# Kernel tuning notes

Measured on AMD Instinct MI355X. Metric: run time of the kernel, lower is better.

The kernel has to match this reference:

```python
import jax, jax.numpy as jnp
import numpy as np

E = 512      # embedding_size
H = 8        # heads
FF = 4 * E   # ffn hidden
EPS = 1e-5


def layer_norm(x, gamma, beta):
    mu = jnp.mean(x, axis=-1, keepdims=True)
    var = jnp.mean((x - mu) ** 2, axis=-1, keepdims=True)
    return (x - mu) * jax.lax.rsqrt(var + EPS) * gamma + beta


def setup_inputs() -> dict:
    key = jax.random.key(0)
    ks = jax.random.split(key, 12)
    N, L = 4, 2048
    s = E ** -0.5
    return {
        "x": jax.random.normal(ks[0], (N, L, E), jnp.float32),
        "wq": jax.random.normal(ks[1], (E, E), jnp.float32) * s,
        "wk": jax.random.normal(ks[2], (E, E), jnp.float32) * s,
        "wv": jax.random.normal(ks[3], (E, E), jnp.float32) * s,
        "wo": jax.random.normal(ks[4], (E, E), jnp.float32) * s,
        "bo": jnp.zeros((E,), jnp.float32),
        "g1": jnp.ones((E,), jnp.float32),
        "b1": jnp.zeros((E,), jnp.float32),
        "g2": jnp.ones((E,), jnp.float32),
        "b2": jnp.zeros((E,), jnp.float32),
        "w1": jax.random.normal(ks[5], (E, FF), jnp.float32) * s,
        "bf1": jnp.zeros((FF,), jnp.float32),
        "w2": jax.random.normal(ks[6], (FF, E), jnp.float32) * (FF ** -0.5),
        "bf2": jnp.zeros((E,), jnp.float32),
    }


def reference(x, wq, wk, wv, wo, bo, g1, b1, g2, b2, w1, bf1, w2, bf2):
    N, L, _ = x.shape
    skip = x
    h = layer_norm(x, g1, b1)
    # attention (weights stored as [in, out])
    q = (h @ wq).reshape(N, L, H, E // H)
    k = (h @ wk).reshape(N, L, H, E // H)
    v = (h @ wv).reshape(N, L, H, E // H)
    # NOTE: source scales by embedding_size**-0.5 (not head_dim)
    scores = jnp.einsum('nqhd,nkhd->nhqk', q, k) * (E ** -0.5)
    attn = jax.nn.softmax(scores, axis=-1)
    out = jnp.einsum('nhql,nlhd->nqhd', attn, v).reshape(N, L, E)
    x = out @ wo + bo + skip
    skip = x
    h = layer_norm(x, g2, b2)  # dropout is identity in eval
    h = jax.nn.silu(h @ w1 + bf1) @ w2 + bf2
    return h + skip
```

## Files before the change

kernel.cpp:

```cpp
#include <hip/hip_runtime.h>
#include <hip/hip_bf16.h>

typedef __bf16 bf16;
typedef __attribute__((ext_vector_type(2))) __bf16 bf16x2;
typedef __attribute__((ext_vector_type(8))) __bf16 bf16x8;
typedef __attribute__((ext_vector_type(4))) float f32x4;
typedef __attribute__((ext_vector_type(16))) float f32x16;

#define MFMA16(a, b, c) __builtin_amdgcn_mfma_f32_16x16x32_bf16((a), (b), (c), 0, 0, 0)
#define MFMA32(a, b, c) __builtin_amdgcn_mfma_f32_32x32x16_bf16((a), (b), (c), 0, 0, 0)


__device__ __forceinline__ void load_lds16(const bf16* g, bf16* l) {
    __builtin_amdgcn_global_load_lds(
        (const __attribute__((address_space(1))) void*)g,
        (__attribute__((address_space(3))) void*)l, 16, 0, 0);
}

__device__ __forceinline__ float fexp2(float x) { return __builtin_amdgcn_exp2f(x); }

__global__ void cvt_all(const float* __restrict__ wq, const float* __restrict__ wk,
                        const float* __restrict__ wv, const float* __restrict__ wo,
                        const float* __restrict__ w1, const float* __restrict__ w2,
                        bf16* __restrict__ wqkv_t, bf16* __restrict__ wo_t,
                        bf16* __restrict__ w1_t, bf16* __restrict__ w2_t) {
    __shared__ float t[64][65];
    const int b = blockIdx.x;
    const float* src; bf16* dst;
    int sstride, dstride, r0, c0, dr0;
    if (b < 192) {
        int bx = b % 24, by = b / 24;
        int j0 = bx * 64;
        src = (j0 < 512) ? wq : (j0 < 1024) ? wk : wv;
        sstride = 512; r0 = by * 64; c0 = j0 & 511;
        dst = wqkv_t; dstride = 512; dr0 = j0;
    } else if (b < 256) {
        int tt = b - 192; int bx = tt % 8, by = tt / 8;
        src = wo; sstride = 512; r0 = by * 64; c0 = bx * 64;
        dst = wo_t; dstride = 512; dr0 = c0;
    } else if (b < 512) {
        int tt = b - 256; int bx = tt % 32, by = tt / 32;
        src = w1; sstride = 2048; r0 = by * 64; c0 = bx * 64;
        dst = w1_t; dstride = 512; dr0 = c0;
    } else {
        int tt = b - 512; int bx = tt % 8, by = tt / 8;
        src = w2; sstride = 512; r0 = by * 64; c0 = bx * 64;
        dst = w2_t; dstride = 2048; dr0 = c0;
    }
    #pragma unroll
    for (int p = 0; p < 16; p++) {
        int lin = threadIdx.x + p * 256;
        int rr = lin >> 6, cc = lin & 63;
        t[rr][cc] = src[(size_t)(r0 + rr) * sstride + c0 + cc];
    }
    __syncthreads();
    #pragma unroll
    for (int p = 0; p < 16; p++) {
        int lin = threadIdx.x + p * 256;
        int cc = lin >> 6, rr = lin & 63;
        dst[(size_t)(dr0 + cc) * dstride + r0 + rr] = (bf16)t[rr][cc];
    }
}

__global__ void ln_kernel(const float* __restrict__ x, const float* __restrict__ g,
                          const float* __restrict__ b, bf16* __restrict__ out) {
    int row = blockIdx.x * 4 + (threadIdx.x >> 6);
    int lane = threadIdx.x & 63;
    const float4* xr = (const float4*)(x + (size_t)row * 512);
    float4 v0 = xr[lane];
    float4 v1 = xr[lane + 64];
    float s  = v0.x + v0.y + v0.z + v0.w + v1.x + v1.y + v1.z + v1.w;
    float sq = v0.x*v0.x + v0.y*v0.y + v0.z*v0.z + v0.w*v0.w
             + v1.x*v1.x + v1.y*v1.y + v1.z*v1.z + v1.w*v1.w;
    #pragma unroll
    for (int d = 1; d < 64; d <<= 1) { s += __shfl_xor(s, d); sq += __shfl_xor(sq, d); }
    float mean = s * (1.f / 512.f);
    float var  = sq * (1.f / 512.f) - mean * mean;
    float rs   = rsqrtf(var + 1e-5f);
    const float4* gv = (const float4*)g;
    const float4* bv = (const float4*)b;
    float4 ga = gv[lane], gb = gv[lane + 64];
    float4 ba = bv[lane], bb = bv[lane + 64];
    bf16* orow = out + (size_t)row * 512;
    int c0 = lane * 4;
    orow[c0 + 0]   = (bf16)((v0.x - mean) * rs * ga.x + ba.x);
    orow[c0 + 1]   = (bf16)((v0.y - mean) * rs * ga.y + ba.y);
    orow[c0 + 2]   = (bf16)((v0.z - mean) * rs * ga.z + ba.z);
    orow[c0 + 3]   = (bf16)((v0.w - mean) * rs * ga.w + ba.w);
    orow[c0 + 256] = (bf16)((v1.x - mean) * rs * gb.x + bb.x);
    orow[c0 + 257] = (bf16)((v1.y - mean) * rs * gb.y + bb.y);
    orow[c0 + 258] = (bf16)((v1.z - mean) * rs * gb.z + bb.z);
    orow[c0 + 259] = (bf16)((v1.w - mean) * rs * gb.w + bb.w);
}

template<int KD, int ND, int EPI>
__global__ __launch_bounds__(256, 3) void gemm_k(
        const bf16* __restrict__ A, const bf16* __restrict__ Bt,
        const float* __restrict__ bias, void* __restrict__ outp) {
    __shared__ bf16 As[128 * 64];
    __shared__ bf16 Bs[128 * 64];
    const int bm = blockIdx.x, bn = blockIdx.y;
    const int tid = threadIdx.x;
    const int w = tid >> 6, lane = tid & 63;
    const int wm = (w >> 1) * 64, wn = (w & 1) * 64;
    const int lr = lane & 15, lq = lane >> 4, lr7 = lane & 7;
    const int srow = lane >> 3, gslot = lane & 7;
    f32x4 acc[4][4] = {};
    const bf16* Ab = A + (size_t)bm * 128 * KD;
    const bf16* Bb = Bt + (size_t)bn * 128 * KD;
    const int gcol = (gslot ^ srow) * 8;
    for (int k0 = 0; k0 < KD; k0 += 64) {
        __syncthreads();
        #pragma unroll
        for (int s = 0; s < 4; s++) {
            int rbase = w * 32 + s * 8;
            int row = rbase + srow;
            load_lds16(&Ab[(size_t)row * KD + k0 + gcol], &As[rbase * 64]);
            load_lds16(&Bb[(size_t)row * KD + k0 + gcol], &Bs[rbase * 64]);
        }
        __syncthreads();
        #pragma unroll
        for (int ks = 0; ks < 2; ks++) {
            bf16x8 af[4], bfr[4];
            #pragma unroll
            for (int mi = 0; mi < 4; mi++) {
                int row = wm + mi * 16 + lr;
                af[mi] = *(const bf16x8*)&As[row * 64 + (((ks * 4 + lq) ^ lr7) << 3)];
            }
            #pragma unroll
            for (int ni = 0; ni < 4; ni++) {
                int row = wn + ni * 16 + lr;
                bfr[ni] = *(const bf16x8*)&Bs[row * 64 + (((ks * 4 + lq) ^ lr7) << 3)];
            }
            #pragma unroll
            for (int mi = 0; mi < 4; mi++)
                #pragma unroll
                for (int ni = 0; ni < 4; ni++)
                    acc[mi][ni] = MFMA16(af[mi], bfr[ni], acc[mi][ni]);
        }
    }
    #pragma unroll
    for (int mi = 0; mi < 4; mi++)
        #pragma unroll
        for (int ni = 0; ni < 4; ni++)
            #pragma unroll
            for (int r = 0; r < 4; r++) {
                int row = bm * 128 + wm + mi * 16 + lq * 4 + r;
                int col = bn * 128 + wn + ni * 16 + lr;
                float v = acc[mi][ni][r];
                size_t off = (size_t)row * ND + col;
                if constexpr (EPI == 0) {
                    ((bf16*)outp)[off] = (bf16)v;
                } else {
                    v += bias[col];
                    v = v / (1.f + __expf(-v));
                    ((bf16*)outp)[off] = (bf16)v;
                }
            }
}

template<int KD>
__global__ __launch_bounds__(256, 4) void gemm64(
        const bf16* __restrict__ A, const bf16* __restrict__ Bt,
        const float* __restrict__ bias, const float* __restrict__ resid,
        float* __restrict__ outp) {
    __shared__ bf16 As[64 * 64];
    __shared__ bf16 Bs[64 * 64];
    const int bm = blockIdx.x, bn = blockIdx.y;
    const int tid = threadIdx.x;
    const int w = tid >> 6, lane = tid & 63;
    const int wm = (w >> 1) * 32, wn = (w & 1) * 32;
    const int lr = lane & 15, lq = lane >> 4, lr7 = lane & 7;
    const int srow = lane >> 3, gslot = lane & 7;
    f32x4 acc[2][2] = {};
    const bf16* Ab = A + (size_t)bm * 64 * KD;
    const bf16* Bb = Bt + (size_t)bn * 64 * KD;
    const int gcol = (gslot ^ srow) * 8;
    for (int k0 = 0; k0 < KD; k0 += 64) {
        __syncthreads();
        #pragma unroll
        for (int s = 0; s < 2; s++) {
            int rbase = w * 16 + s * 8;
            int row = rbase + srow;
            load_lds16(&Ab[(size_t)row * KD + k0 + gcol], &As[rbase * 64]);
            load_lds16(&Bb[(size_t)row * KD + k0 + gcol], &Bs[rbase * 64]);
        }
        __syncthreads();
        #pragma unroll
        for (int ks = 0; ks < 2; ks++) {
            bf16x8 af[2], bfr[2];
            #pragma unroll
            for (int mi = 0; mi < 2; mi++) {
                int row = wm + mi * 16 + lr;
                af[mi] = *(const bf16x8*)&As[row * 64 + (((ks * 4 + lq) ^ lr7) << 3)];
            }
            #pragma unroll
            for (int ni = 0; ni < 2; ni++) {
                int row = wn + ni * 16 + lr;
                bfr[ni] = *(const bf16x8*)&Bs[row * 64 + (((ks * 4 + lq) ^ lr7) << 3)];
            }
            #pragma unroll
            for (int mi = 0; mi < 2; mi++)
                #pragma unroll
                for (int ni = 0; ni < 2; ni++)
                    acc[mi][ni] = MFMA16(af[mi], bfr[ni], acc[mi][ni]);
        }
    }
    #pragma unroll
    for (int mi = 0; mi < 2; mi++)
        #pragma unroll
        for (int ni = 0; ni < 2; ni++)
            #pragma unroll
            for (int r = 0; r < 4; r++) {
                int row = bm * 64 + wm + mi * 16 + lq * 4 + r;
                int col = bn * 64 + wn + ni * 16 + lr;
                size_t off = (size_t)row * 512 + col;
                outp[off] = acc[mi][ni][r] + bias[col] + resid[off];
            }
}

__global__ void vt_kernel(const bf16* __restrict__ qkvb, bf16* __restrict__ Vt) {
    __shared__ bf16 t[64 * 72];
    const int nh = blockIdx.x & 31, lt = blockIdx.x >> 5;
    const int n = nh >> 3, h = nh & 7;
    const int tid = threadIdx.x;
    #pragma unroll
    for (int p = 0; p < 2; p++) {
        int lin = tid + p * 256;
        int rr = lin >> 3, cc = lin & 7;
        bf16x8 v = *(const bf16x8*)&qkvb[(size_t)(n * 2048 + lt * 64 + rr) * 1536
                                         + 1024 + h * 64 + cc * 8];
        *(bf16x8*)&t[rr * 72 + (cc ^ (rr & 7)) * 8] = v;
    }
    __syncthreads();
    #pragma unroll
    for (int p = 0; p < 2; p++) {
        int lin = tid + p * 256;
        int dd = lin & 63, llc = lin >> 6;
        bf16x8 o;
        #pragma unroll
        for (int j = 0; j < 8; j++) {
            int ll = llc * 8 + j;
            o[j] = t[ll * 72 + (((dd >> 3) ^ (ll & 7)) * 8) + (dd & 7)];
        }
        *(bf16x8*)&Vt[(size_t)(nh * 64 + dd) * 2048 + lt * 64 + llc * 8] = o;
    }
}

__global__ __launch_bounds__(512, 4) void attn_kernel(const bf16* __restrict__ qkv,
                                                      const bf16* __restrict__ Vt,
                                                      bf16* __restrict__ aout) {
    __shared__ float accbuf[4][32][64];
    __shared__ float psumbuf[4][32];
    __shared__ bf16 Ot[4][32 * 72];
    const int b = blockIdx.x;
    const int nh = b & 31;
    const int qt = b >> 5;
    const int n = nh >> 3, h = nh & 7;
    const int tid = threadIdx.x, w = tid >> 6, lane = tid & 63;
    const int qsub = w & 3, ks = w >> 2;
    const int lq5 = lane & 31, g = lane >> 5;
    const float cf = 0.04419417382415922f * 1.4426950408889634f;

    const bf16* Qp = qkv + (size_t)(n * 2048 + qt * 128 + qsub * 32 + lq5) * 1536
                     + h * 64 + g * 8;
    bf16x8 qf[4];
    #pragma unroll
    for (int c = 0; c < 4; c++) {
        bf16x8 raw = *(const bf16x8*)(Qp + c * 16);
        #pragma unroll
        for (int j = 0; j < 8; j++) qf[c][j] = (bf16)((float)raw[j] * cf);
    }

    f32x16 acc0 = {0}, acc1 = {0};
    float psum = 0.f;

    const bf16* Kp = qkv + (size_t)(n * 2048 + ks * 1024 + lq5) * 1536
                     + 512 + h * 64 + g * 8;
    const bf16* Vp = Vt + (size_t)(nh * 64 + lq5) * 2048 + ks * 1024 + g * 8;

    bf16x8 kfn[4];
    kfn[0] = *(const bf16x8*)(Kp);
    kfn[1] = *(const bf16x8*)(Kp + 16);
    kfn[2] = *(const bf16x8*)(Kp + 32);
    kfn[3] = *(const bf16x8*)(Kp + 48);

    #pragma unroll 2
    for (int t = 0; t < 32; t++) {
        const bf16* Vc = Vp + t * 32;
        bf16x8 v00 = *(const bf16x8*)(Vc);
        bf16x8 v01 = *(const bf16x8*)(Vc + (size_t)32 * 2048);
        bf16x8 v10 = *(const bf16x8*)(Vc + 16);
        bf16x8 v11 = *(const bf16x8*)(Vc + 16 + (size_t)32 * 2048);

        f32x16 st = {0};
        st = MFMA32(kfn[0], qf[0], st);
        st = MFMA32(kfn[1], qf[1], st);
        st = MFMA32(kfn[2], qf[2], st);
        st = MFMA32(kfn[3], qf[3], st);

        if (t < 31) {
            const bf16* Kt = Kp + (size_t)(t + 1) * 32 * 1536;
            kfn[0] = *(const bf16x8*)(Kt);
            kfn[1] = *(const bf16x8*)(Kt + 16);
            kfn[2] = *(const bf16x8*)(Kt + 32);
            kfn[3] = *(const bf16x8*)(Kt + 48);
        }

        #pragma unroll
        for (int h16 = 0; h16 < 2; h16++) {
            uint32_t pk[4];
            #pragma unroll
            for (int i = 0; i < 4; i++) {
                float p0 = fexp2(fminf(st[8 * h16 + 2 * i], 60.f));
                float p1 = fexp2(fminf(st[8 * h16 + 2 * i + 1], 60.f));
                psum += p0 + p1;
                union { uint32_t u; bf16x2 hh; } cvu;
                cvu.hh = bf16x2{(bf16)p0, (bf16)p1};
                pk[i] = cvu.u;
            }
            uint32_t s0 = g ? pk[0] : pk[2];
            uint32_t s1 = g ? pk[1] : pk[3];
            uint32_t r0 = (uint32_t)__shfl_xor((int)s0, 32);
            uint32_t r1 = (uint32_t)__shfl_xor((int)s1, 32);
            union { uint4 u; bf16x8 v; } pf;
            pf.u = g == 0 ? uint4{pk[0], pk[1], r0, r1}
                          : uint4{r0, r1, pk[2], pk[3]};
            if (h16 == 0) {
                acc0 = MFMA32(v00, pf.v, acc0);
                acc1 = MFMA32(v01, pf.v, acc1);
            } else {
                acc0 = MFMA32(v10, pf.v, acc0);
                acc1 = MFMA32(v11, pf.v, acc1);
            }
        }
    }

    float tot = psum + __shfl_xor(psum, 32);

    if (ks == 1) {
        #pragma unroll
        for (int r = 0; r < 16; r++) {
            accbuf[qsub][r][lane]      = acc0[r];
            accbuf[qsub][16 + r][lane] = acc1[r];
        }
        if (g == 0) psumbuf[qsub][lq5] = tot;
    }
    __syncthreads();
    if (ks == 0) {
        float inv = 1.f / (tot + psumbuf[qsub][lq5]);
        bf16* ot = Ot[qsub];
        #pragma unroll
        for (int r = 0; r < 16; r++) {
            float a0 = acc0[r] + accbuf[qsub][r][lane];
            float a1 = acc1[r] + accbuf[qsub][16 + r][lane];
            int d0 = (r & 3) + 8 * (r >> 2) + 4 * g;
            ot[lq5 * 72 + d0]      = (bf16)(a0 * inv);
            ot[lq5 * 72 + d0 + 32] = (bf16)(a1 * inv);
        }
        __builtin_amdgcn_s_waitcnt(0);
        #pragma unroll
        for (int i = 0; i < 4; i++) {
            int tq = i * 8 + (lane >> 3);
            bf16x8 ov = *(const bf16x8*)&ot[tq * 72 + (lane & 7) * 8];
            *(bf16x8*)&aout[(size_t)(n * 2048 + qt * 128 + qsub * 32 + tq) * 512
                            + h * 64 + (lane & 7) * 8] = ov;
        }
    }
}

extern "C" void kernel_launch(void* const* d_in, const int* in_sizes, int n_in,
                              void* d_out, int out_size, void* d_ws, size_t ws_size,
                              hipStream_t stream) {
    (void)in_sizes; (void)n_in; (void)out_size; (void)ws_size;
    const float* x   = (const float*)d_in[0];
    const float* wq  = (const float*)d_in[1];
    const float* wk  = (const float*)d_in[2];
    const float* wv  = (const float*)d_in[3];
    const float* wo  = (const float*)d_in[4];
    const float* bo  = (const float*)d_in[5];
    const float* g1  = (const float*)d_in[6];
    const float* b1  = (const float*)d_in[7];
    const float* g2  = (const float*)d_in[8];
    const float* b2  = (const float*)d_in[9];
    const float* w1  = (const float*)d_in[10];
    const float* bf1 = (const float*)d_in[11];
    const float* w2  = (const float*)d_in[12];
    const float* bf2 = (const float*)d_in[13];
    float* out = (float*)d_out;

    char* p = (char*)d_ws;
    bf16*  h1     = (bf16*)p;  p += (size_t)8192 * 512 * 2;
    bf16*  qkvb   = (bf16*)p;  p += (size_t)8192 * 1536 * 2;
    bf16*  aout   = (bf16*)p;  p += (size_t)8192 * 512 * 2;
    float* x2     = (float*)p; p += (size_t)8192 * 512 * 4;
    bf16*  ff1    = (bf16*)p;  p += (size_t)8192 * 2048 * 2;
    bf16*  wqkv_t = (bf16*)p;  p += (size_t)1536 * 512 * 2;
    bf16*  wo_t   = (bf16*)p;  p += (size_t)512 * 512 * 2;
    bf16*  w1_t   = (bf16*)p;  p += (size_t)2048 * 512 * 2;
    bf16*  w2_t   = (bf16*)p;  p += (size_t)512 * 2048 * 2;
    bf16*  Vt     = (bf16*)ff1;

    cvt_all<<<768, 256, 0, stream>>>(wq, wk, wv, wo, w1, w2, wqkv_t, wo_t, w1_t, w2_t);

    ln_kernel<<<2048, 256, 0, stream>>>(x, g1, b1, h1);
    gemm_k<512, 1536, 0><<<dim3(64, 12), 256, 0, stream>>>(h1, wqkv_t, nullptr, qkvb);
    vt_kernel<<<1024, 256, 0, stream>>>(qkvb, Vt);
    attn_kernel<<<512, 512, 0, stream>>>(qkvb, Vt, aout);
    gemm64<512><<<dim3(128, 8), 256, 0, stream>>>(aout, wo_t, bo, x, x2);
    ln_kernel<<<2048, 256, 0, stream>>>(x2, g2, b2, h1);
    gemm_k<512, 2048, 2><<<dim3(64, 16), 256, 0, stream>>>(h1, w1_t, bf1, ff1);
    gemm64<2048><<<dim3(128, 8), 256, 0, stream>>>(ff1, w2_t, bf2, x2, out);
}
```

Before: 303.0 us.

## Pre-pack K and V into MFMA fragment order for coalesced attention loads

The V-transpose kernel becomes a pack kernel that writes both K and V into a fragment-major layout, so each wave's 64 lanes read one contiguous 1 KB chunk per MFMA operand. The attention loop previously read K with a 3 KB row stride from the fused QKV buffer and V with strided rows. Coalescing these loads should cut memory transactions in the attention inner loop. In exchange, the pack kernel does extra work writing K, and both packed buffers are placed in the ff1 scratch area.

```diff
diff --git a/kernel.cpp b/kernel.cpp
--- a/kernel.cpp
+++ b/kernel.cpp
@@ -219,11 +219,23 @@
             }
 }
 
-__global__ void vt_kernel(const bf16* __restrict__ qkvb, bf16* __restrict__ Vt) {
+__global__ void pack_kv(const bf16* __restrict__ qkvb, bf16* __restrict__ Kfrag,
+                        bf16* __restrict__ Vfrag) {
     __shared__ bf16 t[64 * 72];
     const int nh = blockIdx.x & 31, lt = blockIdx.x >> 5;
     const int n = nh >> 3, h = nh & 7;
     const int tid = threadIdx.x;
+    #pragma unroll
+    for (int p = 0; p < 2; p++) {
+        int cid = tid + p * 256;
+        int key = lt * 64 + (cid >> 3);
+        int dc = cid & 7;
+        bf16x8 kv = *(const bf16x8*)&qkvb[(size_t)(n * 2048 + key) * 1536
+                                          + 512 + h * 64 + dc * 8];
+        int kb = key >> 5, l5 = key & 31;
+        int c = dc >> 1, g = dc & 1;
+        *(bf16x8*)&Kfrag[(size_t)(((nh * 64 + kb) * 4 + c) * 64 + g * 32 + l5) * 8] = kv;
+    }
     #pragma unroll
     for (int p = 0; p < 2; p++) {
         int lin = tid + p * 256;
@@ -236,19 +248,25 @@
     #pragma unroll
     for (int p = 0; p < 2; p++) {
         int lin = tid + p * 256;
-        int dd = lin & 63, llc = lin >> 6;
+        int dd = lin & 63, llc = lin >> 6 | (p << 2);
         bf16x8 o;
         #pragma unroll
         for (int j = 0; j < 8; j++) {
             int ll = llc * 8 + j;
             o[j] = t[ll * 72 + (((dd >> 3) ^ (ll & 7)) * 8) + (dd & 7)];
         }
-        *(bf16x8*)&Vt[(size_t)(nh * 64 + dd) * 2048 + lt * 64 + llc * 8] = o;
+        int token0 = lt * 64 + llc * 8;
+        int kb = token0 >> 5;
+        int tl5 = token0 & 31;
+        int r = ((tl5 >> 4) << 1) | (dd >> 5);
+        int lane = ((token0 >> 3) & 1) * 32 + (dd & 31);
+        *(bf16x8*)&Vfrag[(size_t)(((nh * 64 + kb) * 4 + r) * 64 + lane) * 8] = o;
     }
 }
 
 __global__ __launch_bounds__(512, 4) void attn_kernel(const bf16* __restrict__ qkv,
-                                                      const bf16* __restrict__ Vt,
+                                                      const bf16* __restrict__ Kfrag,
+                                                      const bf16* __restrict__ Vfrag,
                                                       bf16* __restrict__ aout) {
     __shared__ float accbuf[4][32][64];
     __shared__ float psumbuf[4][32];
@@ -275,23 +293,22 @@
     f32x16 acc0 = {0}, acc1 = {0};
     float psum = 0.f;
 
-    const bf16* Kp = qkv + (size_t)(n * 2048 + ks * 1024 + lq5) * 1536
-                     + 512 + h * 64 + g * 8;
-    const bf16* Vp = Vt + (size_t)(nh * 64 + lq5) * 2048 + ks * 1024 + g * 8;
+    const bf16* Kb = Kfrag + (size_t)((nh * 64 + ks * 32) * 4) * 512 + lane * 8;
+    const bf16* Vb = Vfrag + (size_t)((nh * 64 + ks * 32) * 4) * 512 + lane * 8;
 
     bf16x8 kfn[4];
-    kfn[0] = *(const bf16x8*)(Kp);
-    kfn[1] = *(const bf16x8*)(Kp + 16);
-    kfn[2] = *(const bf16x8*)(Kp + 32);
-    kfn[3] = *(const bf16x8*)(Kp + 48);
+    kfn[0] = *(const bf16x8*)(Kb);
+    kfn[1] = *(const bf16x8*)(Kb + 512);
+    kfn[2] = *(const bf16x8*)(Kb + 1024);
+    kfn[3] = *(const bf16x8*)(Kb + 1536);
 
     #pragma unroll 2
     for (int t = 0; t < 32; t++) {
-        const bf16* Vc = Vp + t * 32;
+        const bf16* Vc = Vb + t * 2048;
         bf16x8 v00 = *(const bf16x8*)(Vc);
-        bf16x8 v01 = *(const bf16x8*)(Vc + (size_t)32 * 2048);
-        bf16x8 v10 = *(const bf16x8*)(Vc + 16);
-        bf16x8 v11 = *(const bf16x8*)(Vc + 16 + (size_t)32 * 2048);
+        bf16x8 v01 = *(const bf16x8*)(Vc + 512);
+        bf16x8 v10 = *(const bf16x8*)(Vc + 1024);
+        bf16x8 v11 = *(const bf16x8*)(Vc + 1536);
 
         f32x16 st = {0};
         st = MFMA32(kfn[0], qf[0], st);
@@ -300,11 +317,11 @@
         st = MFMA32(kfn[3], qf[3], st);
 
         if (t < 31) {
-            const bf16* Kt = Kp + (size_t)(t + 1) * 32 * 1536;
+            const bf16* Kt = Kb + (t + 1) * 2048;
             kfn[0] = *(const bf16x8*)(Kt);
-            kfn[1] = *(const bf16x8*)(Kt + 16);
-            kfn[2] = *(const bf16x8*)(Kt + 32);
-            kfn[3] = *(const bf16x8*)(Kt + 48);
+            kfn[1] = *(const bf16x8*)(Kt + 512);
+            kfn[2] = *(const bf16x8*)(Kt + 1024);
+            kfn[3] = *(const bf16x8*)(Kt + 1536);
         }
 
         #pragma unroll
@@ -399,14 +416,15 @@
     bf16*  wo_t   = (bf16*)p;  p += (size_t)512 * 512 * 2;
     bf16*  w1_t   = (bf16*)p;  p += (size_t)2048 * 512 * 2;
     bf16*  w2_t   = (bf16*)p;  p += (size_t)512 * 2048 * 2;
-    bf16*  Vt     = (bf16*)ff1;
+    bf16*  Kfrag  = (bf16*)ff1;
+    bf16*  Vfrag  = Kfrag + (size_t)8192 * 512;
 
     cvt_all<<<768, 256, 0, stream>>>(wq, wk, wv, wo, w1, w2, wqkv_t, wo_t, w1_t, w2_t);
 
     ln_kernel<<<2048, 256, 0, stream>>>(x, g1, b1, h1);
     gemm_k<512, 1536, 0><<<dim3(64, 12), 256, 0, stream>>>(h1, wqkv_t, nullptr, qkvb);
-    vt_kernel<<<1024, 256, 0, stream>>>(qkvb, Vt);
-    attn_kernel<<<512, 512, 0, stream>>>(qkvb, Vt, aout);
+    pack_kv<<<1024, 256, 0, stream>>>(qkvb, Kfrag, Vfrag);
+    attn_kernel<<<512, 512, 0, stream>>>(qkvb, Kfrag, Vfrag, aout);
     gemm64<512><<<dim3(128, 8), 256, 0, stream>>>(aout, wo_t, bo, x, x2);
     ln_kernel<<<2048, 256, 0, stream>>>(x2, g2, b2, h1);
     gemm_k<512, 2048, 2><<<dim3(64, 16), 256, 0, stream>>>(h1, w1_t, bf1, ff1);
```

Measured after the change: 243.7 us. 1.24x faster.
